# Performance work log

Hardware: AMD Instinct MI355X
Metric: run time of the kernel (lower is better)

## Reference

```python
import jax, jax.numpy as jnp
import numpy as np
from jax import lax

NL, H, E, N, R, K, C, V, P = 8, 768, 1536, 16, 4, 4, 3, 256, 2048
EPS = 1e-5

def layernorm(x, w, b):
    m = jnp.mean(x, -1, keepdims=True)
    v = jnp.var(x, -1, keepdims=True)
    return (x - m) * lax.rsqrt(v + EPS) * w + b

def causal_dwconv(x, w, b):
    # x: [B,L,E], w: [E,K], b: [E]; causal depthwise conv (pad K-1 left, truncate)
    Bn, L, _ = x.shape
    xp = jnp.pad(x, ((0, 0), (K - 1, 0), (0, 0)))
    y = b
    acc = jnp.zeros_like(x)
    for j in range(K):
        acc = acc + xp[:, j:j + L, :] * w[:, j]
    return acc + b

def selective_scan(u, dt, Bm, Cm, A, Dv):
    # u,dt: [B,L,E]; Bm,Cm: [B,L,N]; A: [E,N]; Dv: [E]
    Bn = u.shape[0]
    def step(h, inp):
        u_t, dt_t, b_t, c_t = inp  # [B,E],[B,E],[B,N],[B,N]
        dA = jnp.exp(dt_t[:, :, None] * A)                      # [B,E,N]
        h = h * dA + (dt_t * u_t)[:, :, None] * b_t[:, None, :]
        y = jnp.einsum('ben,bn->be', h, c_t)
        return h, y
    h0 = jnp.zeros((Bn, E, N), dtype=u.dtype)
    xs = (u.transpose(1, 0, 2), dt.transpose(1, 0, 2),
          Bm.transpose(1, 0, 2), Cm.transpose(1, 0, 2))
    _, ys = lax.scan(step, h0, xs)
    return ys.transpose(1, 0, 2) + u * Dv

def mamba_block(hs, p):
    res = hs
    x = layernorm(hs, p['ln_w'], p['ln_b'])
    proj = x @ p['in_w'] + p['in_b']                            # [B,L,2E]
    xm, gate = proj[..., :E], proj[..., E:]
    xm = causal_dwconv(xm, p['conv_w'], p['conv_b'])
    u = jax.nn.silu(xm)                                         # swish activation in mixer
    dbc = u @ p['xproj_w']                                      # [B,L,R+2N]
    dt = jax.nn.softplus(dbc[..., :R] @ p['dt_w'] + p['dt_b'])  # [B,L,E]
    Bm, Cm = dbc[..., R:R + N], dbc[..., R + N:]
    A = -jnp.exp(p['A_log'])                                    # [E,N]
    y = selective_scan(u, dt, Bm, Cm, A, p['D'])
    y = jax.nn.sigmoid(gate) * y
    hs = y @ p['out_w'] + p['out_b'] + res
    # fractal layer: mean of recursive swish-linear branches, residual
    acc = jnp.zeros_like(hs)
    for i in range(C):
        yb = hs
        for _ in range(3):
            yb = jax.nn.silu(yb @ p['frac_w'][i] + p['frac_b'][i])
        acc = acc + yb
    return hs + 0.5 * acc / C

def setup_inputs() -> dict:
    key = jax.random.key(0)
    ks = jax.random.split(key, 20)
    s = lambda i, shp, sc=0.02: jax.random.normal(ks[i], shp, jnp.float32) * sc
    inp = {
        'input_ids': jax.random.randint(ks[0], (2, 2048), 0, V),
        'tok_emb': s(1, (V, H)),
        'pos_emb': s(2, (P, H)),
        'ln_w': jnp.ones((NL, H)), 'ln_b': jnp.zeros((NL, H)),
        'in_w': s(3, (NL, H, 2 * E)), 'in_b': jnp.zeros((NL, 2 * E)),
        'conv_w': s(4, (NL, E, K), 0.3), 'conv_b': jnp.zeros((NL, E)),
        'xproj_w': s(5, (NL, E, R + 2 * N)),
        'dt_w': s(6, (NL, R, E), 0.1),
        'dt_b': jnp.full((NL, E), -4.0),
        'A_log': jnp.tile(jnp.log(jnp.arange(1, N + 1, dtype=jnp.float32)), (NL, E, 1)),
        'D': jnp.ones((NL, E)),
        'out_w': s(7, (NL, E, H)), 'out_b': jnp.zeros((NL, H)),
        'frac_w': s(8, (NL, C, H, H)), 'frac_b': jnp.zeros((NL, C, H)),
        'fln_w': jnp.ones((H,)), 'fln_b': jnp.zeros((H,)),
    }
    return inp

def reference(input_ids, tok_emb, pos_emb, ln_w, ln_b, in_w, in_b, conv_w, conv_b,
              xproj_w, dt_w, dt_b, A_log, D, out_w, out_b, frac_w, frac_b, fln_w, fln_b):
    Bn, L = input_ids.shape
    hs = tok_emb[input_ids] + pos_emb[jnp.arange(L)][None]
    for l in range(NL):
        p = {'ln_w': ln_w[l], 'ln_b': ln_b[l], 'in_w': in_w[l], 'in_b': in_b[l],
             'conv_w': conv_w[l], 'conv_b': conv_b[l], 'xproj_w': xproj_w[l],
             'dt_w': dt_w[l], 'dt_b': dt_b[l], 'A_log': A_log[l], 'D': D[l],
             'out_w': out_w[l], 'out_b': out_b[l], 'frac_w': frac_w[l], 'frac_b': frac_b[l]}
        hs = mamba_block(hs, p)
    return layernorm(hs, fln_w, fln_b)
```

## Files before the change

kernel.cpp:

```cpp
#include <hip/hip_runtime.h>
#include <hip/hip_bf16.h>
#include <stdint.h>

#define NLAYER 8
#define HDIM   768
#define EDIM   1536
#define NST    16
#define LSEQ   2048
#define BATCH  2
#define BLTOK  (BATCH*LSEQ)
#define NCH    (BATCH*EDIM)
#define NCHK   64

typedef unsigned short u16;
typedef short  short8  __attribute__((ext_vector_type(8)));
typedef float  f32x4   __attribute__((ext_vector_type(4)));
typedef unsigned short u16x4 __attribute__((ext_vector_type(4)));

__device__ __forceinline__ float sigm(float x){ return 1.0f/(1.0f+__expf(-x)); }

__device__ __forceinline__ u16 bf16_rne(float x){
  unsigned u = __float_as_uint(x);
  return (u16)((u + 0x7fffu + ((u>>16)&1u)) >> 16);
}
__device__ __forceinline__ float bf16_f(u16 h){
  return __uint_as_float(((unsigned)h)<<16);
}

__device__ __forceinline__ void gload16(const void* g, void* l){
  __builtin_amdgcn_global_load_lds(
    reinterpret_cast<const __attribute__((address_space(1))) unsigned*>(
        reinterpret_cast<uintptr_t>(g)),
    reinterpret_cast<__attribute__((address_space(3))) unsigned*>(
        reinterpret_cast<uintptr_t>(l)),
    16, 0, 0);
}

__global__ __launch_bounds__(256) void wprep_k(
    const float* __restrict__ W, u16* __restrict__ H, u16* __restrict__ L,
    int Nsrc, int Ndst, int K)
{
  __shared__ float T[32][33];
  int z = blockIdx.z;
  W += (size_t)z*K*Nsrc; H += (size_t)z*Ndst*K; L += (size_t)z*Ndst*K;
  int n0 = blockIdx.x*32, k0 = blockIdx.y*32;
  int tx = threadIdx.x&31, ty = threadIdx.x>>5;
  #pragma unroll
  for (int r=0;r<4;r++){
    int kk = ty+8*r, col = n0+tx;
    T[kk][tx] = (col<Nsrc) ? W[(size_t)(k0+kk)*Nsrc+col] : 0.f;
  }
  __syncthreads();
  #pragma unroll
  for (int r=0;r<4;r++){
    int nn = ty+8*r, n = n0+nn, k = k0+tx;
    if (n<Ndst){
      float f = T[tx][nn];
      u16 h = bf16_rne(f);
      H[(size_t)n*K+k] = h;
      L[(size_t)n*K+k] = bf16_rne(f - bf16_f(h));
    }
  }
}

template<int EPI, int SPLIT, int SPLITK>
__global__ __launch_bounds__(256) void gemm_u(
    const u16* __restrict__ AH, const u16* __restrict__ AL, int lda,
    const u16* __restrict__ WH, const u16* __restrict__ WL, int ldw,
    const float* __restrict__ bias, void* __restrict__ Cout,
    int N, int Kloop, size_t zA, size_t zW, size_t zB, size_t zC)
{
  constexpr int NPL = (SPLIT==3)?4:2;
  constexpr int NLD = (SPLIT==3)?8:4;
  __shared__ __align__(16) u16 smem[2*NPL*4096];

  const int z = blockIdx.z;
  const u16* ah = AH + (size_t)z*zA;
  const u16* bh = WH + (size_t)z*zW;
  const u16* al = nullptr;
  const u16* bl = nullptr;
  if constexpr (SPLIT==3){ al = AL + (size_t)z*zA; bl = WL + (size_t)z*zW; }

  const int tid  = threadIdx.x;
  const int m0 = blockIdx.y<<7, n0 = blockIdx.x<<7;
  const int wave = tid>>6, lane = tid&63;
  const int r = lane&15, q = lane>>4;
  const int wm = (wave&1)<<6, wn = (wave>>1)<<6;
  const int srow = tid>>2;
  const int scol = (tid&3)*8;
  const int sdst = tid*8;

  const int nk = Kloop >> 5;

  auto STAGE = [&](int idx){
    u16* s = smem + (size_t)(idx&1)*NPL*4096;
    const int k0 = idx<<5;
    #pragma unroll
    for (int i=0;i<2;i++){
      const size_t gao = (size_t)(m0 + i*64 + srow)*lda + k0 + scol;
      const size_t gbo = (size_t)(n0 + i*64 + srow)*ldw + k0 + scol;
      const int lo = i*2048 + sdst;
      gload16(ah+gao, s+lo);
      gload16(bh+gbo, s+4096+lo);
      if constexpr (SPLIT==3){
        gload16(al+gao, s+2*4096+lo);
        gload16(bl+gbo, s+3*4096+lo);
      }
    }
  };

  f32x4 acc[4][4];
  #pragma unroll
  for (int i=0;i<4;i++)
    #pragma unroll
    for (int j=0;j<4;j++)
      #pragma unroll
      for (int t=0;t<4;t++) acc[i][j][t]=0.f;

  STAGE(0);
  if (nk > 1) STAGE(1);

  for (int idx = 0; idx < nk; idx++){
    if (idx+1 < nk) asm volatile("s_waitcnt vmcnt(%0)" :: "n"(NLD) : "memory");
    else            asm volatile("s_waitcnt vmcnt(0)" ::: "memory");
    __builtin_amdgcn_s_barrier();

    const u16* s = smem + (size_t)(idx&1)*NPL*4096;
    const u16* sA = s;
    const u16* sB = s + 4096;

    short8 aHf[4], bHf[4];
    #pragma unroll
    for (int i=0;i<4;i++) aHf[i] = *(const short8*)&sA[(wm + 16*i + r)*32 + q*8];
    #pragma unroll
    for (int j=0;j<4;j++) bHf[j] = *(const short8*)&sB[(wn + 16*j + r)*32 + q*8];
    short8 aLf[4], bLf[4];
    if constexpr (SPLIT==3){
      const u16* sAL = s + 2*4096;
      const u16* sBL = s + 3*4096;
      #pragma unroll
      for (int i=0;i<4;i++) aLf[i] = *(const short8*)&sAL[(wm + 16*i + r)*32 + q*8];
      #pragma unroll
      for (int j=0;j<4;j++) bLf[j] = *(const short8*)&sBL[(wn + 16*j + r)*32 + q*8];
    }
    asm volatile("s_waitcnt lgkmcnt(0)" ::: "memory");
    __builtin_amdgcn_sched_barrier(0);
    __builtin_amdgcn_s_barrier();

    if (idx+2 < nk) STAGE(idx+2);

    if constexpr (SPLIT==3){
      #pragma unroll
      for (int i=0;i<4;i++)
        #pragma unroll
        for (int j=0;j<4;j++){
          acc[i][j] = __builtin_amdgcn_mfma_f32_16x16x32_bf16(aHf[i], bHf[j], acc[i][j], 0,0,0);
          acc[i][j] = __builtin_amdgcn_mfma_f32_16x16x32_bf16(aHf[i], bLf[j], acc[i][j], 0,0,0);
          acc[i][j] = __builtin_amdgcn_mfma_f32_16x16x32_bf16(aLf[i], bHf[j], acc[i][j], 0,0,0);
        }
    } else {
      #pragma unroll
      for (int i=0;i<4;i++)
        #pragma unroll
        for (int j=0;j<4;j++)
          acc[i][j] = __builtin_amdgcn_mfma_f32_16x16x32_bf16(aHf[i], bHf[j], acc[i][j], 0,0,0);
    }
  }

  float* Cf = (float*)Cout + (size_t)z*zC;
  u16*   Cu = (u16*)Cout   + (size_t)z*zC;
  const float* bz = bias ? (bias + (size_t)z*zB) : bias;
  #pragma unroll
  for (int j=0;j<4;j++){
    int n_out = n0 + wn + 16*j + r;
    float bv = (bz && (!SPLITK || z==0)) ? bz[n_out] : 0.f;
    #pragma unroll
    for (int i=0;i<4;i++){
      #pragma unroll
      for (int reg=0;reg<4;reg++){
        int m_out = m0 + wm + 16*i + 4*q + reg;
        float v = acc[i][j][reg] + bv;
        if (EPI & 1)  v *= sigm(v);
        if (EPI & 32) v *= (0.5f/3.0f);
        size_t o = (size_t)m_out*N + n_out;
        if      (EPI & 16) atomicAdd(&Cf[o], v);
        else if (EPI & 8)  Cu[o] = bf16_rne(v);
        else if (EPI & 2)  Cf[o] += v;
        else               Cf[o] = v;
      }
    }
  }
}

__global__ __launch_bounds__(256) void xgemm_k(
    const float* __restrict__ A, const u16* __restrict__ XH,
    const u16* __restrict__ XL, float* __restrict__ DBC)
{
  __shared__ f32x4 red[3][4][64];
  int m0 = blockIdx.x*16;
  int wv = threadIdx.x>>6, lane = threadIdx.x&63;
  int r = lane&15, q = lane>>4;
  f32x4 acc[3];
  #pragma unroll
  for (int j=0;j<3;j++)
    #pragma unroll
    for (int t=0;t<4;t++) acc[j][t]=0.f;

  const int KW = EDIM/4;
  const int kend = (wv+1)*KW;
  for (int k0 = wv*KW; k0 < kend; k0 += 32){
    const float* ap = A + (size_t)(m0+r)*EDIM + k0 + q*8;
    float f[8];
    *(float4*)&f[0] = *(const float4*)(ap+0);
    *(float4*)&f[4] = *(const float4*)(ap+4);
    short8 ah, al;
    #pragma unroll
    for (int t=0;t<8;t++){
      u16 h = bf16_rne(f[t]);
      ah[t] = (short)h;
      al[t] = (short)bf16_rne(f[t]-bf16_f(h));
    }
    #pragma unroll
    for (int j=0;j<3;j++){
      size_t o = (size_t)(16*j+r)*EDIM + k0 + q*8;
      short8 bh = *(const short8*)&XH[o];
      short8 bl = *(const short8*)&XL[o];
      acc[j] = __builtin_amdgcn_mfma_f32_16x16x32_bf16(ah, bh, acc[j], 0,0,0);
      acc[j] = __builtin_amdgcn_mfma_f32_16x16x32_bf16(ah, bl, acc[j], 0,0,0);
      acc[j] = __builtin_amdgcn_mfma_f32_16x16x32_bf16(al, bh, acc[j], 0,0,0);
    }
  }
  #pragma unroll
  for (int j=0;j<3;j++) red[j][wv][lane] = acc[j];
  __syncthreads();
  if (wv == 0){
    #pragma unroll
    for (int j=0;j<3;j++){
      f32x4 s = red[j][0][lane];
      s += red[j][1][lane];
      s += red[j][2][lane];
      s += red[j][3][lane];
      int n = 16*j + r;
      if (n < 36){
        #pragma unroll
        for (int reg=0;reg<4;reg++){
          int m = m0 + 4*q + reg;
          DBC[(size_t)m*36 + n] = s[reg];
        }
      }
    }
  }
}

__global__ __launch_bounds__(256) void embed_k(
    const int* __restrict__ ids, const float* __restrict__ tok,
    const float* __restrict__ pos, float* __restrict__ HS)
{
  int idx = blockIdx.x*256 + threadIdx.x;
  int h = idx % HDIM; int t = idx / HDIM;
  int lpos = t % LSEQ;
  int id = ids[t];
  HS[idx] = tok[id*HDIM + h] + pos[lpos*HDIM + h];
}

template<int PACK>
__global__ __launch_bounds__(256) void ln_k(
    const float* __restrict__ X, const float* __restrict__ w,
    const float* __restrict__ b, void* __restrict__ O1, void* __restrict__ O2)
{
  int wv = threadIdx.x>>6, lane = threadIdx.x&63;
  int t = blockIdx.x*4 + wv;
  const float* x = X + (size_t)t*HDIM;
  float v[12];
  float s=0.f, s2=0.f;
  #pragma unroll
  for (int k=0;k<12;k++){
    v[k] = x[lane + 64*k];
    s += v[k]; s2 += v[k]*v[k];
  }
  #pragma unroll
  for (int off=32; off; off>>=1){
    s  += __shfl_xor(s,  off, 64);
    s2 += __shfl_xor(s2, off, 64);
  }
  float m = s/HDIM, rr = rsqrtf(s2/HDIM - m*m + 1e-5f);
  #pragma unroll
  for (int k=0;k<12;k++){
    int i = lane + 64*k;
    float o = (v[k]-m)*rr*w[i] + b[i];
    if (PACK){
      u16 h = bf16_rne(o);
      ((u16*)O1)[(size_t)t*HDIM+i] = h;
      ((u16*)O2)[(size_t)t*HDIM+i] = bf16_rne(o - bf16_f(h));
    } else {
      ((float*)O1)[(size_t)t*HDIM+i] = o;
    }
  }
}

__global__ __launch_bounds__(256) void cvt_k(
    const float* __restrict__ X, u16* __restrict__ O)
{
  int i = blockIdx.x*256 + threadIdx.x;
  float4 v = ((const float4*)X)[i];
  u16x4 o;
  o[0]=bf16_rne(v.x); o[1]=bf16_rne(v.y); o[2]=bf16_rne(v.z); o[3]=bf16_rne(v.w);
  ((u16x4*)O)[i] = o;
}

__global__ __launch_bounds__(256) void conv_silu_k(
    const float* __restrict__ PROJ, const float* __restrict__ cw,
    const float* __restrict__ cb, float* __restrict__ U)
{
  int idx = blockIdx.x*256 + threadIdx.x;
  int e = idx % EDIM; int t = idx / EDIM;
  int l = t % LSEQ; int tb = t - l;
  float acc = cb[e];
  #pragma unroll
  for (int j=0;j<4;j++){
    int tt = l + j - 3;
    if (tt >= 0) acc += PROJ[(size_t)(tb+tt)*(2*EDIM) + e] * cw[e*4+j];
  }
  U[idx] = acc * sigm(acc);
}

__global__ __launch_bounds__(256) void scanA_k(
    const float* __restrict__ U, const float* __restrict__ DBC,
    const float* __restrict__ Alog, const float* __restrict__ dtw,
    const float* __restrict__ dtb, float* __restrict__ PSP,
    float* __restrict__ PSS)
{
  const int CH = LSEQ/NCHK;
  int el = threadIdx.x & 63, jj = threadIdx.x >> 6;
  int ch = blockIdx.x*64 + el;
  int j  = blockIdx.y*4 + jj;
  int e = ch % EDIM, b = ch / EDIM;

  float a[16], P[16], S[16];
  #pragma unroll
  for (int n=0;n<16;n++){ a[n] = -__expf(Alog[e*NST+n]); P[n]=1.f; S[n]=0.f; }
  float w0=dtw[e], w1=dtw[EDIM+e], w2=dtw[2*EDIM+e], w3=dtw[3*EDIM+e];
  float db=dtb[e];
  size_t base=(size_t)b*LSEQ;

  for (int t=j*CH; t<j*CH+CH; t++){
    size_t tok = base+t;
    float4 d4 = *(const float4*)&DBC[tok*36];
    float4 B0 = *(const float4*)&DBC[tok*36+4];
    float4 B1 = *(const float4*)&DBC[tok*36+8];
    float4 B2 = *(const float4*)&DBC[tok*36+12];
    float4 B3 = *(const float4*)&DBC[tok*36+16];
    float dt = d4.x*w0 + d4.y*w1 + d4.z*w2 + d4.w*w3 + db;
    dt = (dt>20.f)?dt:log1pf(__expf(dt));
    float du = dt * U[tok*EDIM+e];
    float Bv[16];
    *(float4*)&Bv[0]=B0; *(float4*)&Bv[4]=B1; *(float4*)&Bv[8]=B2; *(float4*)&Bv[12]=B3;
    #pragma unroll
    for (int n=0;n<16;n++){
      float dA = __expf(dt*a[n]);
      P[n]*=dA; S[n]=S[n]*dA + du*Bv[n];
    }
  }
  #pragma unroll
  for (int n=0;n<16;n++){
    PSP[(size_t)(j*16+n)*NCH + ch] = P[n];
    PSS[(size_t)(j*16+n)*NCH + ch] = S[n];
  }
}

__global__ __launch_bounds__(256) void scanB_k(
    const float* __restrict__ PSP, float* __restrict__ PSS)
{
  int idx = blockIdx.x*256 + threadIdx.x;
  int n = idx / NCH, ch = idx % NCH;
  float hin = 0.f;
  #pragma unroll 4
  for (int jj=0;jj<NCHK;jj++){
    size_t o = (size_t)(jj*16+n)*NCH + ch;
    float p = PSP[o], s = PSS[o];
    PSS[o] = hin;
    hin = p*hin + s;
  }
}

__global__ __launch_bounds__(256) void scanC_k(
    const float* __restrict__ U, const float* __restrict__ DBC,
    const float* __restrict__ Alog, const float* __restrict__ dtw,
    const float* __restrict__ dtb, const float* __restrict__ HIN,
    const float* __restrict__ Dp, const float* __restrict__ PROJ,
    u16* __restrict__ YH, u16* __restrict__ YL)
{
  const int CH = LSEQ/NCHK;
  int el = threadIdx.x & 63, jj = threadIdx.x >> 6;
  int ch = blockIdx.x*64 + el;
  int j  = blockIdx.y*4 + jj;
  int e = ch % EDIM, b = ch / EDIM;

  float a[16], h[16];
  #pragma unroll
  for (int n=0;n<16;n++){
    a[n] = -__expf(Alog[e*NST+n]);
    h[n] = HIN[(size_t)(j*16+n)*NCH + ch];
  }
  float w0=dtw[e], w1=dtw[EDIM+e], w2=dtw[2*EDIM+e], w3=dtw[3*EDIM+e];
  float db=dtb[e], dcf=Dp[e];
  size_t base=(size_t)b*LSEQ;

  for (int t=j*CH; t<j*CH+CH; t++){
    size_t tok = base+t;
    float4 d4 = *(const float4*)&DBC[tok*36];
    float4 B0 = *(const float4*)&DBC[tok*36+4];
    float4 B1 = *(const float4*)&DBC[tok*36+8];
    float4 B2 = *(const float4*)&DBC[tok*36+12];
    float4 B3 = *(const float4*)&DBC[tok*36+16];
    float4 C0 = *(const float4*)&DBC[tok*36+20];
    float4 C1 = *(const float4*)&DBC[tok*36+24];
    float4 C2 = *(const float4*)&DBC[tok*36+28];
    float4 C3 = *(const float4*)&DBC[tok*36+32];
    float dt = d4.x*w0 + d4.y*w1 + d4.z*w2 + d4.w*w3 + db;
    dt = (dt>20.f)?dt:log1pf(__expf(dt));
    float u = U[tok*EDIM+e];
    float du = dt * u;
    float Bv[16], Cv[16];
    *(float4*)&Bv[0]=B0; *(float4*)&Bv[4]=B1; *(float4*)&Bv[8]=B2; *(float4*)&Bv[12]=B3;
    *(float4*)&Cv[0]=C0; *(float4*)&Cv[4]=C1; *(float4*)&Cv[8]=C2; *(float4*)&Cv[12]=C3;
    float y = 0.f;
    #pragma unroll
    for (int n=0;n<16;n++){
      float dA = __expf(dt*a[n]);
      h[n] = h[n]*dA + du*Bv[n];
      y += h[n]*Cv[n];
    }
    float g = PROJ[tok*(2*EDIM) + EDIM + e];
    float yv = (y + u*dcf)*sigm(g);
    u16 hh = bf16_rne(yv);
    YH[tok*EDIM + e] = hh;
    YL[tok*EDIM + e] = bf16_rne(yv - bf16_f(hh));
  }
}

extern "C" void kernel_launch(void* const* d_in, const int* in_sizes, int n_in,
                              void* d_out, int out_size, void* d_ws, size_t ws_size,
                              hipStream_t stream)
{
  const int*   ids      = (const int*)d_in[0];
  const float* tok_emb  = (const float*)d_in[1];
  const float* pos_emb  = (const float*)d_in[2];
  const float* ln_w     = (const float*)d_in[3];
  const float* ln_b     = (const float*)d_in[4];
  const float* in_w     = (const float*)d_in[5];
  const float* in_b     = (const float*)d_in[6];
  const float* conv_w   = (const float*)d_in[7];
  const float* conv_b   = (const float*)d_in[8];
  const float* xproj_w  = (const float*)d_in[9];
  const float* dt_w     = (const float*)d_in[10];
  const float* dt_b     = (const float*)d_in[11];
  const float* A_log    = (const float*)d_in[12];
  const float* Dp       = (const float*)d_in[13];
  const float* out_w    = (const float*)d_in[14];
  const float* out_b    = (const float*)d_in[15];
  const float* frac_w   = (const float*)d_in[16];
  const float* frac_b   = (const float*)d_in[17];
  const float* fln_w    = (const float*)d_in[18];
  const float* fln_b    = (const float*)d_in[19];

  const size_t F_HS   = (size_t)BLTOK*HDIM;
  const size_t F_PROJ = (size_t)BLTOK*2*EDIM;
  const size_t F_R1   = (size_t)BLTOK*EDIM;
  float* HS   = (float*)d_ws;
  float* PROJ = HS   + F_HS;
  float* R1   = PROJ + F_PROJ;
  float* DBC  = R1   + F_R1;
  u16* W16  = (u16*)(DBC + (size_t)BLTOK*36);
  u16* inH  = W16;
  u16* inL  = inH  + (size_t)2359296;
  u16* outH = inL  + (size_t)2359296;
  u16* outL = outH + (size_t)1179648;
  u16* frH  = outL + (size_t)1179648;
  u16* frL  = frH  + (size_t)1769472;
  u16* xH   = frL  + (size_t)1769472;
  u16* xL   = xH   + (size_t)73728;
  float* PSP = (float*)(xL + (size_t)73728);
  float* PSS = PSP + (size_t)NCHK*16*NCH;
  u16* YH  = (u16*)(PSS + (size_t)NCHK*16*NCH);
  u16* YL  = YH + (size_t)BLTOK*EDIM;
  u16*   XH  = (u16*)R1;
  u16*   XL  = XH + F_HS;
  float* U   = R1;
  u16*   HSB = (u16*)PSP;
  u16*   S1  = (u16*)(PROJ + 3*F_HS);
  u16*   S2  = S1 + 3*F_HS;

  embed_k<<<(BLTOK*HDIM)/256, 256, 0, stream>>>(ids, tok_emb, pos_emb, HS);

  const size_t zWf = (size_t)HDIM*HDIM;
  for (int l = 0; l < NLAYER; l++){
    wprep_k<<<dim3(3072/32, 768/32), 256, 0, stream>>>(
        in_w + (size_t)l*HDIM*2*EDIM, inH, inL, 2*EDIM, 2*EDIM, HDIM);
    wprep_k<<<dim3(768/32, 1536/32), 256, 0, stream>>>(
        out_w + (size_t)l*EDIM*HDIM, outH, outL, HDIM, HDIM, EDIM);
    wprep_k<<<dim3(768/32, 768/32, 3), 256, 0, stream>>>(
        frac_w + (size_t)l*3*HDIM*HDIM, frH, frL, HDIM, HDIM, HDIM);
    wprep_k<<<dim3(2, 1536/32), 256, 0, stream>>>(
        xproj_w + (size_t)l*EDIM*36, xH, xL, 36, 48, EDIM);

    ln_k<1><<<BLTOK/4, 256, 0, stream>>>(HS, ln_w + l*HDIM, ln_b + l*HDIM, XH, XL);

    gemm_u<0,3,0><<<dim3(24, 32), 256, 0, stream>>>(
        XH, XL, HDIM, inH, inL, HDIM, in_b + l*2*EDIM, PROJ,
        2*EDIM, HDIM, 0,0,0,0);

    conv_silu_k<<<(BLTOK*EDIM)/256, 256, 0, stream>>>(
        PROJ, conv_w + l*EDIM*4, conv_b + l*EDIM, U);

    xgemm_k<<<BLTOK/16, 256, 0, stream>>>(U, xH, xL, DBC);

    scanA_k<<<dim3(NCH/64, NCHK/4), 256, 0, stream>>>(
        U, DBC, A_log + (size_t)l*EDIM*NST, dt_w + (size_t)l*4*EDIM,
        dt_b + (size_t)l*EDIM, PSP, PSS);
    scanB_k<<<(NCH*16)/256, 256, 0, stream>>>(PSP, PSS);
    scanC_k<<<dim3(NCH/64, NCHK/4), 256, 0, stream>>>(
        U, DBC, A_log + (size_t)l*EDIM*NST, dt_w + (size_t)l*4*EDIM,
        dt_b + (size_t)l*EDIM, PSS, Dp + (size_t)l*EDIM, PROJ, YH, YL);

    gemm_u<16,3,1><<<dim3(6, 32, 2), 256, 0, stream>>>(
        YH, YL, EDIM, outH, outL, EDIM, out_b + l*HDIM, HS,
        HDIM, EDIM/2, EDIM/2, EDIM/2, 0, 0);

    cvt_k<<<(BLTOK*HDIM)/1024, 256, 0, stream>>>(HS, HSB);

    gemm_u<9,1,0><<<dim3(6, 32, 3), 256, 0, stream>>>(
        HSB, nullptr, HDIM, frH, frL, HDIM, frac_b + (size_t)l*3*HDIM, S1,
        HDIM, HDIM, 0, zWf, HDIM, F_HS);
    gemm_u<9,1,0><<<dim3(6, 32, 3), 256, 0, stream>>>(
        S1, nullptr, HDIM, frH, frL, HDIM, frac_b + (size_t)l*3*HDIM, S2,
        HDIM, HDIM, F_HS, zWf, HDIM, F_HS);
    gemm_u<1|16|32,1,0><<<dim3(6, 32, 3), 256, 0, stream>>>(
        S2, nullptr, HDIM, frH, frL, HDIM, frac_b + (size_t)l*3*HDIM, HS,
        HDIM, HDIM, F_HS, zWf, HDIM, 0);
  }

  ln_k<0><<<BLTOK/4, 256, 0, stream>>>(HS, fln_w, fln_b, (float*)d_out, nullptr);
}
```

Before: 3.547 ms.

## Merge per-layer weight-prep launches, swizzle GEMM tiles, raise out-proj split-K to four

The four per-layer weight split/transposition launches become a single kernel that picks its matrix from the flat block index, which cuts launch overhead and tail effects. GEMM workgroups are remapped with a stride-8 swizzle over the tile grid to change the order tiles run in, aiming at better L2 locality. The out-projection split-K goes from 2 to 4 slices, giving more workgroups in exchange for more atomic or partial-sum traffic into HS. The swizzle assumes the workgroup count is a multiple of 8, which holds for these grids.

Result: no change. 3.510 ms (-1.1%).

```diff
diff --git a/kernel.cpp b/kernel.cpp
--- a/kernel.cpp
+++ b/kernel.cpp
@@ -36,14 +36,27 @@
     16, 0, 0);
 }
 
-__global__ __launch_bounds__(256) void wprep_k(
-    const float* __restrict__ W, u16* __restrict__ H, u16* __restrict__ L,
-    int Nsrc, int Ndst, int K)
+__global__ __launch_bounds__(256) void wprep4_k(
+    const float* __restrict__ Win,  u16* __restrict__ inH,  u16* __restrict__ inL,
+    const float* __restrict__ Wout, u16* __restrict__ outH, u16* __restrict__ outL,
+    const float* __restrict__ Wfr,  u16* __restrict__ frH,  u16* __restrict__ frL,
+    const float* __restrict__ Wxp,  u16* __restrict__ xH,   u16* __restrict__ xL)
 {
   __shared__ float T[32][33];
-  int z = blockIdx.z;
-  W += (size_t)z*K*Nsrc; H += (size_t)z*Ndst*K; L += (size_t)z*Ndst*K;
-  int n0 = blockIdx.x*32, k0 = blockIdx.y*32;
+  int id = blockIdx.x;
+  const float* W; u16 *H; u16 *L; int Nsrc, Ndst, K, bx, by;
+  if (id < 2304){
+    W=Win; H=inH; L=inL; Nsrc=3072; Ndst=3072; K=768; bx=id%96; by=id/96;
+  } else if (id < 3456){
+    id-=2304; W=Wout; H=outH; L=outL; Nsrc=768; Ndst=768; K=1536; bx=id%24; by=id/24;
+  } else if (id < 5184){
+    id-=3456; int z=id/576; id-=z*576;
+    W=Wfr+(size_t)z*589824; H=frH+(size_t)z*589824; L=frL+(size_t)z*589824;
+    Nsrc=768; Ndst=768; K=768; bx=id%24; by=id/24;
+  } else {
+    id-=5184; W=Wxp; H=xH; L=xL; Nsrc=36; Ndst=48; K=1536; bx=id%2; by=id/2;
+  }
+  int n0 = bx*32, k0 = by*32;
   int tx = threadIdx.x&31, ty = threadIdx.x>>5;
   #pragma unroll
   for (int r=0;r<4;r++){
@@ -81,8 +94,17 @@
   const u16* bl = nullptr;
   if constexpr (SPLIT==3){ al = AL + (size_t)z*zA; bl = WL + (size_t)z*zW; }
 
+  int bx, by;
+  {
+    const int nx = gridDim.x, nwg = nx*gridDim.y;
+    int id = blockIdx.x + nx*blockIdx.y;
+    const int q = nwg >> 3;
+    int swz = (id & 7)*q + (id >> 3);
+    bx = swz % nx; by = swz / nx;
+  }
+
   const int tid  = threadIdx.x;
-  const int m0 = blockIdx.y<<7, n0 = blockIdx.x<<7;
+  const int m0 = by<<7, n0 = bx<<7;
   const int wave = tid>>6, lane = tid&63;
   const int r = lane&15, q = lane>>4;
   const int wm = (wave&1)<<6, wn = (wave>>1)<<6;
@@ -495,14 +517,11 @@
 
   const size_t zWf = (size_t)HDIM*HDIM;
   for (int l = 0; l < NLAYER; l++){
-    wprep_k<<<dim3(3072/32, 768/32), 256, 0, stream>>>(
-        in_w + (size_t)l*HDIM*2*EDIM, inH, inL, 2*EDIM, 2*EDIM, HDIM);
-    wprep_k<<<dim3(768/32, 1536/32), 256, 0, stream>>>(
-        out_w + (size_t)l*EDIM*HDIM, outH, outL, HDIM, HDIM, EDIM);
-    wprep_k<<<dim3(768/32, 768/32, 3), 256, 0, stream>>>(
-        frac_w + (size_t)l*3*HDIM*HDIM, frH, frL, HDIM, HDIM, HDIM);
-    wprep_k<<<dim3(2, 1536/32), 256, 0, stream>>>(
-        xproj_w + (size_t)l*EDIM*36, xH, xL, 36, 48, EDIM);
+    wprep4_k<<<5280, 256, 0, stream>>>(
+        in_w   + (size_t)l*HDIM*2*EDIM, inH, inL,
+        out_w  + (size_t)l*EDIM*HDIM,  outH, outL,
+        frac_w + (size_t)l*3*HDIM*HDIM, frH, frL,
+        xproj_w+ (size_t)l*EDIM*36,    xH,  xL);
 
     ln_k<1><<<BLTOK/4, 256, 0, stream>>>(HS, ln_w + l*HDIM, ln_b + l*HDIM, XH, XL);
 
@@ -523,9 +542,9 @@
         U, DBC, A_log + (size_t)l*EDIM*NST, dt_w + (size_t)l*4*EDIM,
         dt_b + (size_t)l*EDIM, PSS, Dp + (size_t)l*EDIM, PROJ, YH, YL);
 
-    gemm_u<16,3,1><<<dim3(6, 32, 2), 256, 0, stream>>>(
+    gemm_u<16,3,1><<<dim3(6, 32, 4), 256, 0, stream>>>(
         YH, YL, EDIM, outH, outL, EDIM, out_b + l*HDIM, HS,
-        HDIM, EDIM/2, EDIM/2, EDIM/2, 0, 0);
+        HDIM, EDIM/4, EDIM/4, EDIM/4, 0, 0);
 
     cvt_k<<<(BLTOK*HDIM)/1024, 256, 0, stream>>>(HS, HSB);
 
```
